# Kernel tuning notes

Hardware: AMD Instinct MI355X
Metric: run time of the kernel (lower is better)

The kernel has to match this reference:

```python
import math
import jax, jax.numpy as jnp
import numpy as np

BATCH, DEPTH = 16, 12
N_NODES = 2 ** DEPTH - 1  # 4095, heap layout: children of i are 2i+1, 2i+2
IN_F, OUT_F, STATE_F = 512, 512, 256


def setup_inputs() -> dict:
    key = jax.random.key(0)
    ks = jax.random.split(key, 10)
    x_batch = jax.random.normal(ks[0], (BATCH, N_NODES, IN_F), dtype=jnp.float32)
    idx_batch = jnp.arange(BATCH, dtype=jnp.int32)
    W_in = jax.random.normal(ks[1], (IN_F, IN_F), dtype=jnp.float32) / math.sqrt(IN_F)
    b_in = jnp.zeros((IN_F,), dtype=jnp.float32)
    u1 = jax.random.uniform(ks[2], (STATE_F,), dtype=jnp.float32)
    u2 = jax.random.uniform(ks[3], (STATE_F,), dtype=jnp.float32)
    nu_log = jnp.log(-0.5 * jnp.log(u1 + 1e-6))
    theta_log = jnp.log(2.0 * math.pi * u2)
    lam_mod = jnp.exp(-jnp.exp(nu_log))
    gamma_log = jnp.log(jnp.sqrt(1.0 - jnp.square(lam_mod)))
    B_re = jax.random.normal(ks[4], (STATE_F, IN_F), dtype=jnp.float32) / math.sqrt(2 * IN_F)
    B_im = jax.random.normal(ks[5], (STATE_F, IN_F), dtype=jnp.float32) / math.sqrt(2 * IN_F)
    C_re = jax.random.normal(ks[6], (OUT_F, STATE_F), dtype=jnp.float32) / math.sqrt(STATE_F)
    C_im = jax.random.normal(ks[7], (OUT_F, STATE_F), dtype=jnp.float32) / math.sqrt(STATE_F)
    return dict(x_batch=x_batch, idx_batch=idx_batch, W_in=W_in, b_in=b_in,
                nu_log=nu_log, theta_log=theta_log, gamma_log=gamma_log,
                B_re=B_re, B_im=B_im, C_re=C_re, C_im=C_im)


def reference(x_batch, idx_batch, W_in, b_in, nu_log, theta_log, gamma_log,
              B_re, B_im, C_re, C_im):
    bsz, n_nodes, _ = x_batch.shape
    depth = int(round(math.log2(n_nodes + 1)))
    S = B_re.shape[0]

    # LRU constants (complex lambda kept as (re, im) pair)
    lam_mod = jnp.exp(-jnp.exp(nu_log))           # [S]
    th = jnp.exp(theta_log)
    lr, li = lam_mod * jnp.cos(th), lam_mod * jnp.sin(th)
    gamma = jnp.exp(gamma_log)                    # [S]

    proj = x_batch @ W_in.T + b_in                # [B, N, IN]
    # complex input term (proj is real): proj @ B^T
    in_re = jnp.einsum('bni,si->bns', proj, B_re) # [B, N, S]
    in_im = jnp.einsum('bni,si->bns', proj, B_im)

    h_re = jnp.zeros((bsz, n_nodes, S), dtype=proj.dtype)
    h_im = jnp.zeros((bsz, n_nodes, S), dtype=proj.dtype)

    # process levels bottom-up; level d nodes occupy [2^d-1, 2^{d+1}-1)
    for d in range(depth - 1, -1, -1):
        a, b = 2 ** d - 1, 2 ** (d + 1) - 1
        n = b - a
        if d == depth - 1:  # leaves: left/right = -1 -> zero child state
            cr = jnp.zeros((bsz, n, S), dtype=proj.dtype)
            ci = jnp.zeros((bsz, n, S), dtype=proj.dtype)
        else:
            # children of nodes [a, b) are the contiguous block [2a+1, 2b+1)
            cr = h_re[:, 2 * a + 1:2 * b + 1].reshape(bsz, n, 2, S).sum(axis=2)
            ci = h_im[:, 2 * a + 1:2 * b + 1].reshape(bsz, n, 2, S).sum(axis=2)
        hr = lr * cr - li * ci + gamma * in_re[:, a:b]
        hi = lr * ci + li * cr + gamma * in_im[:, a:b]
        h_re = h_re.at[:, a:b].set(hr)
        h_im = h_im.at[:, a:b].set(hi)

    # y = Re(h @ C^T), computed once on final states (same math as per-level scatter)
    outputs = jnp.einsum('bns,os->bno', h_re, C_re) - jnp.einsum('bns,os->bno', h_im, C_im)
    return outputs
```

## Files before the change

kernel.cpp:

```cpp
#include <hip/hip_runtime.h>


#define ROWS 65520
#define KDIM 512

typedef __attribute__((ext_vector_type(8))) short bf16x8;
typedef __attribute__((ext_vector_type(4))) float f32x4;

__device__ __forceinline__ unsigned short f2bf(float f) {
    unsigned int u = __float_as_uint(f);
    unsigned int r = (u + 0x7FFFu + ((u >> 16) & 1u)) >> 16;
    return (unsigned short)r;
}
__device__ __forceinline__ float b2f(unsigned short h) {
    return __uint_as_float(((unsigned int)h) << 16);
}

#define CVT_BLKS  32760
#define PM_BASE   32760
#define PC_BASE   33784
#define PB_BASE   34808
#define PREP_GRID 34936

__global__ __launch_bounds__(256) void prep_all(const float* __restrict__ x,
                                                unsigned short* __restrict__ x16,
                                                const float* __restrict__ W,
                                                const float* __restrict__ Bre,
                                                const float* __restrict__ Bim,
                                                const float* __restrict__ gamma_log,
                                                unsigned short* __restrict__ M16,
                                                const float* __restrict__ bin,
                                                float* __restrict__ biasc,
                                                const float* __restrict__ Cre,
                                                const float* __restrict__ Cim,
                                                unsigned short* __restrict__ C16) {
    __shared__ float Bs[16][17];
    __shared__ float Ws[16][17];
    const int blk = blockIdx.x;
    const int t = threadIdx.x;

    if (blk < CVT_BLKS) {
        int i = blk * 256 + t;
        float4 v = ((const float4*)x)[i];
        ushort4 o;
        o.x = f2bf(v.x); o.y = f2bf(v.y); o.z = f2bf(v.z); o.w = f2bf(v.w);
        ((ushort4*)x16)[i] = o;
    } else if (blk < PC_BASE) {
        const int pm = blk - PM_BASE;
        const int bx = pm & 31;
        const int by = pm >> 5;
        const int tx = t & 15;
        const int ty = t >> 4;
        const int j  = bx * 16 + tx;
        const int cc = by * 16 + ty;
        const float* Bsel = (cc < 256) ? (Bre + (size_t)cc * 512)
                                       : (Bim + (size_t)(cc - 256) * 512);
        float acc = 0.f;
        for (int kt = 0; kt < 512; kt += 16) {
            Bs[ty][tx] = Bsel[kt + tx];
            Ws[ty][tx] = W[(size_t)(kt + ty) * 512 + j];
            __syncthreads();
#pragma unroll
            for (int k = 0; k < 16; ++k) acc += Bs[ty][k] * Ws[k][tx];
            __syncthreads();
        }
        float g = expf(gamma_log[cc & 255]);
        M16[(size_t)cc * 512 + j] = f2bf(acc * g);
    } else if (blk < PB_BASE) {
        int idx = (blk - PC_BASE) * 256 + t;
        int o = idx >> 9;
        int s = idx & 511;
        float v = (s < 256) ? Cre[(size_t)o * 256 + s] : -Cim[(size_t)o * 256 + (s - 256)];
        C16[idx] = f2bf(v);
    } else {
        const int c = (blk - PB_BASE) * 4 + (t >> 6);
        const int lane = t & 63;
        const float* Bsel = (c < 256) ? (Bre + (size_t)c * 512)
                                      : (Bim + (size_t)(c - 256) * 512);
        float acc = 0.f;
#pragma unroll
        for (int i = lane; i < 512; i += 64) acc += bin[i] * Bsel[i];
#pragma unroll
        for (int off = 32; off > 0; off >>= 1) acc += __shfl_down(acc, off, 64);
        if (lane == 0) biasc[c] = acc * expf(gamma_log[c & 255]);
    }
}

template <bool OUT_BF16>
__global__ __launch_bounds__(256) void gemm_mfma(const unsigned short* __restrict__ A,
                                                 const unsigned short* __restrict__ Bm,
                                                 const float* __restrict__ bias,
                                                 void* __restrict__ Cout,
                                                 int Mrows) {
    __shared__ __align__(16) unsigned short As[2][128 * 64];
    __shared__ __align__(16) unsigned short Bs[2][128 * 64];
    const int t = threadIdx.x;
    const int lane = t & 63;
    const int w = t >> 6;
    const int wr = (w >> 1) * 64;
    const int wc = (w & 1) * 64;
    const int bid = blockIdx.x;
    const int xcd = bid & 7;
    const int lid = bid >> 3;
    const int rowblk = xcd * 64 + (lid >> 2);
    const int colblk = lid & 3;
    const int row0 = rowblk * 128;
    const int col0 = colblk * 128;
    const int kt0  = (rowblk & 7) * 64;

    f32x4 acc[4][4] = {};

#define STAGE(pb, itv)                                                         \
    do {                                                                       \
        const int kt_ = (kt0 + (itv) * 64) & 511;                              \
        _Pragma("unroll")                                                      \
        for (int q = 0; q < 4; ++q) {                                          \
            int c_   = q * 256 + t;                                            \
            int row_ = c_ >> 3;                                                \
            int kc_  = c_ & 7;                                                 \
            int kg_  = kc_ ^ (row_ & 7);                                       \
            int ar_  = row0 + row_; if (ar_ >= Mrows) ar_ = Mrows - 1;         \
            const unsigned short* ga_ = A + (size_t)ar_ * KDIM + kt_ + kg_ * 8;\
            __builtin_amdgcn_global_load_lds(                                  \
                (const __attribute__((address_space(1))) unsigned int*)ga_,    \
                (__attribute__((address_space(3))) unsigned int*)(&As[pb][c_ * 8]),\
                16, 0, 0);                                                     \
            const unsigned short* gb_ = Bm + (size_t)(col0 + row_) * KDIM + kt_ + kg_ * 8;\
            __builtin_amdgcn_global_load_lds(                                  \
                (const __attribute__((address_space(1))) unsigned int*)gb_,    \
                (__attribute__((address_space(3))) unsigned int*)(&Bs[pb][c_ * 8]),\
                16, 0, 0);                                                     \
        }                                                                      \
    } while (0)

    STAGE(0, 0);
    __syncthreads();

    int cur = 0;
    for (int it = 0; it < 8; ++it) {
        if (it < 7) STAGE(cur ^ 1, it + 1);
#pragma unroll
        for (int kk = 0; kk < 64; kk += 32) {
            const int kgc = kk >> 3;
            bf16x8 af[4], bfr[4];
#pragma unroll
            for (int i = 0; i < 4; ++i) {
                int row = wr + i * 16 + (lane & 15);
                int kca = (kgc + (lane >> 4)) ^ (row & 7);
                af[i] = *(const bf16x8*)(&As[cur][row * 64 + kca * 8]);
                int colr = wc + i * 16 + (lane & 15);
                int kcb = (kgc + (lane >> 4)) ^ (colr & 7);
                bfr[i] = *(const bf16x8*)(&Bs[cur][colr * 64 + kcb * 8]);
            }
#pragma unroll
            for (int i = 0; i < 4; ++i)
#pragma unroll
                for (int j = 0; j < 4; ++j)
                    acc[i][j] = __builtin_amdgcn_mfma_f32_16x16x32_bf16(
                        af[i], bfr[j], acc[i][j], 0, 0, 0);
        }
        __syncthreads();
        cur ^= 1;
    }
#undef STAGE

    const int cq = lane >> 4;
    const int cl = lane & 15;
#pragma unroll
    for (int i = 0; i < 4; ++i) {
#pragma unroll
        for (int j = 0; j < 4; ++j) {
#pragma unroll
            for (int r = 0; r < 4; ++r) {
                int grow = row0 + wr + i * 16 + cq * 4 + r;
                int gcol = col0 + wc + j * 16 + cl;
                if (grow < Mrows) {
                    float v = acc[i][j][r];
                    if (bias) v += bias[gcol];
                    if (OUT_BF16)
                        ((unsigned short*)Cout)[(size_t)grow * 512 + gcol] = f2bf(v);
                    else
                        ((float*)Cout)[(size_t)grow * 512 + gcol] = v;
                }
            }
        }
    }
}

template <int E>
__global__ __launch_bounds__(256) void tree_up(unsigned short* __restrict__ buf,
                                               const float* __restrict__ nu_log,
                                               const float* __restrict__ theta_log,
                                               int root_base) {
    const int b = blockIdx.x;
    const int rs = root_base + blockIdx.y;
    const int c = threadIdx.x;
    constexpr int LEAVES = 1 << E;
    const float lam = expf(-expf(nu_log[c]));
    const float th  = expf(theta_log[c]);
    const float lr  = lam * cosf(th);
    const float li  = lam * sinf(th);
    const size_t base = (size_t)b * 4095;

    float vr[LEAVES], vi[LEAVES];
    {
        const int nbL = ((rs + 1) << E) - 1;
#pragma unroll
        for (int i = 0; i < LEAVES; ++i) {
            const size_t r = (base + nbL + i) * 512;
            vr[i] = b2f(buf[r + c]);
            vi[i] = b2f(buf[r + 256 + c]);
        }
    }
    float gr[LEAVES - 1], gi[LEAVES - 1];
    {
        int idx = 0;
#pragma unroll
        for (int e = E - 1; e >= 0; --e) {
            const int n  = 1 << e;
            const int nb = ((rs + 1) << e) - 1;
#pragma unroll
            for (int i = 0; i < n; ++i) {
                const size_t r = (base + nb + i) * 512;
                gr[idx] = b2f(buf[r + c]);
                gi[idx] = b2f(buf[r + 256 + c]);
                ++idx;
            }
        }
    }
    {
        int idx = 0;
#pragma unroll
        for (int e = E - 1; e >= 0; --e) {
            const int n  = 1 << e;
            const int nb = ((rs + 1) << e) - 1;
#pragma unroll
            for (int i = 0; i < n; ++i) {
                const float cr = vr[2 * i] + vr[2 * i + 1];
                const float ci = vi[2 * i] + vi[2 * i + 1];
                const float hr = lr * cr - li * ci + gr[idx];
                const float hi = lr * ci + li * cr + gi[idx];
                ++idx;
                const size_t r = (base + nb + i) * 512;
                buf[r + c]       = f2bf(hr);
                buf[r + 256 + c] = f2bf(hi);
                vr[i] = hr;
                vi[i] = hi;
            }
        }
    }
}

extern "C" void kernel_launch(void* const* d_in, const int* in_sizes, int n_in,
                              void* d_out, int out_size, void* d_ws, size_t ws_size,
                              hipStream_t stream) {
    const float* x         = (const float*)d_in[0];
    const float* W_in      = (const float*)d_in[2];
    const float* b_in      = (const float*)d_in[3];
    const float* nu_log    = (const float*)d_in[4];
    const float* theta_log = (const float*)d_in[5];
    const float* gamma_log = (const float*)d_in[6];
    const float* B_re      = (const float*)d_in[7];
    const float* B_im      = (const float*)d_in[8];
    const float* C_re      = (const float*)d_in[9];
    const float* C_im      = (const float*)d_in[10];
    float* out = (float*)d_out;

    char* ws = (char*)d_ws;
    const size_t HB = (size_t)ROWS * 512 * 2;
    unsigned short* x16   = (unsigned short*)ws;
    unsigned short* hb16  = (unsigned short*)(ws + HB);
    unsigned short* M16   = (unsigned short*)(ws + 2 * HB);
    unsigned short* C16   = (unsigned short*)(ws + 2 * HB + 512 * 512 * 2);
    float*          biasc = (float*)(ws + 2 * HB + 2 * 512 * 512 * 2);

    prep_all<<<PREP_GRID, 256, 0, stream>>>(x, x16, W_in, B_re, B_im, gamma_log,
                                            M16, b_in, biasc, C_re, C_im, C16);

    gemm_mfma<true><<<2048, 256, 0, stream>>>(x16, M16, biasc, hb16, ROWS);

    tree_up<4><<<dim3(16, 128), 256, 0, stream>>>(hb16, nu_log, theta_log, 127);
    tree_up<4><<<dim3(16, 8),   256, 0, stream>>>(hb16, nu_log, theta_log, 7);
    tree_up<3><<<dim3(16, 1),   256, 0, stream>>>(hb16, nu_log, theta_log, 0);

    gemm_mfma<false><<<2048, 256, 0, stream>>>(hb16, C16, nullptr, out, ROWS);
}
```

Measured before the change: 413.5 us.

## Vectorize tree scan loads, grid-stride x conversion, hoist GEMM addresses, setprio

```diff
diff --git a/kernel.cpp b/kernel.cpp
--- a/kernel.cpp
+++ b/kernel.cpp
@@ -15,12 +15,19 @@
 __device__ __forceinline__ float b2f(unsigned short h) {
     return __uint_as_float(((unsigned int)h) << 16);
 }
-
-#define CVT_BLKS  32760
-#define PM_BASE   32760
-#define PC_BASE   33784
-#define PB_BASE   34808
-#define PREP_GRID 34936
+__device__ __forceinline__ float b2f_lo(unsigned int p) {
+    return __uint_as_float(p << 16);
+}
+__device__ __forceinline__ float b2f_hi(unsigned int p) {
+    return __uint_as_float(p & 0xFFFF0000u);
+}
+
+#define PC_BASE   1024
+#define PB_BASE   2048
+#define CVT_BASE  2176
+#define CVT_BLKS  2048
+#define PREP_GRID 4224
+#define CVT_N4    8386560
 
 __global__ __launch_bounds__(256) void prep_all(const float* __restrict__ x,
                                                 unsigned short* __restrict__ x16,
@@ -39,16 +46,9 @@
     const int blk = blockIdx.x;
     const int t = threadIdx.x;
 
-    if (blk < CVT_BLKS) {
-        int i = blk * 256 + t;
-        float4 v = ((const float4*)x)[i];
-        ushort4 o;
-        o.x = f2bf(v.x); o.y = f2bf(v.y); o.z = f2bf(v.z); o.w = f2bf(v.w);
-        ((ushort4*)x16)[i] = o;
-    } else if (blk < PC_BASE) {
-        const int pm = blk - PM_BASE;
-        const int bx = pm & 31;
-        const int by = pm >> 5;
+    if (blk < PC_BASE) {
+        const int bx = blk & 31;
+        const int by = blk >> 5;
         const int tx = t & 15;
         const int ty = t >> 4;
         const int j  = bx * 16 + tx;
@@ -72,7 +72,7 @@
         int s = idx & 511;
         float v = (s < 256) ? Cre[(size_t)o * 256 + s] : -Cim[(size_t)o * 256 + (s - 256)];
         C16[idx] = f2bf(v);
-    } else {
+    } else if (blk < CVT_BASE) {
         const int c = (blk - PB_BASE) * 4 + (t >> 6);
         const int lane = t & 63;
         const float* Bsel = (c < 256) ? (Bre + (size_t)c * 512)
@@ -83,6 +83,15 @@
 #pragma unroll
         for (int off = 32; off > 0; off >>= 1) acc += __shfl_down(acc, off, 64);
         if (lane == 0) biasc[c] = acc * expf(gamma_log[c & 255]);
+    } else {
+        int i = (blk - CVT_BASE) * 256 + t;
+#pragma unroll 4
+        for (; i < CVT_N4; i += CVT_BLKS * 256) {
+            float4 v = ((const float4*)x)[i];
+            ushort4 o;
+            o.x = f2bf(v.x); o.y = f2bf(v.y); o.z = f2bf(v.z); o.w = f2bf(v.w);
+            ((ushort4*)x16)[i] = o;
+        }
     }
 }
 
@@ -110,25 +119,33 @@
 
     f32x4 acc[4][4] = {};
 
+    const unsigned short* gaB[4];
+    const unsigned short* gbB[4];
+    int ldsoff[4];
+#pragma unroll
+    for (int q = 0; q < 4; ++q) {
+        int c_   = q * 256 + t;
+        int row_ = c_ >> 3;
+        int kc_  = c_ & 7;
+        int kg_  = kc_ ^ (row_ & 7);
+        int ar_  = row0 + row_; if (ar_ >= Mrows) ar_ = Mrows - 1;
+        gaB[q] = A + (size_t)ar_ * KDIM + kg_ * 8;
+        gbB[q] = Bm + (size_t)(col0 + row_) * KDIM + kg_ * 8;
+        ldsoff[q] = c_ * 8;
+    }
+
 #define STAGE(pb, itv)                                                         \
     do {                                                                       \
         const int kt_ = (kt0 + (itv) * 64) & 511;                              \
         _Pragma("unroll")                                                      \
         for (int q = 0; q < 4; ++q) {                                          \
-            int c_   = q * 256 + t;                                            \
-            int row_ = c_ >> 3;                                                \
-            int kc_  = c_ & 7;                                                 \
-            int kg_  = kc_ ^ (row_ & 7);                                       \
-            int ar_  = row0 + row_; if (ar_ >= Mrows) ar_ = Mrows - 1;         \
-            const unsigned short* ga_ = A + (size_t)ar_ * KDIM + kt_ + kg_ * 8;\
             __builtin_amdgcn_global_load_lds(                                  \
-                (const __attribute__((address_space(1))) unsigned int*)ga_,    \
-                (__attribute__((address_space(3))) unsigned int*)(&As[pb][c_ * 8]),\
+                (const __attribute__((address_space(1))) unsigned int*)(gaB[q] + kt_),\
+                (__attribute__((address_space(3))) unsigned int*)(&As[pb][ldsoff[q]]),\
                 16, 0, 0);                                                     \
-            const unsigned short* gb_ = Bm + (size_t)(col0 + row_) * KDIM + kt_ + kg_ * 8;\
             __builtin_amdgcn_global_load_lds(                                  \
-                (const __attribute__((address_space(1))) unsigned int*)gb_,    \
-                (__attribute__((address_space(3))) unsigned int*)(&Bs[pb][c_ * 8]),\
+                (const __attribute__((address_space(1))) unsigned int*)(gbB[q] + kt_),\
+                (__attribute__((address_space(3))) unsigned int*)(&Bs[pb][ldsoff[q]]),\
                 16, 0, 0);                                                     \
         }                                                                      \
     } while (0)
@@ -139,6 +156,7 @@
     int cur = 0;
     for (int it = 0; it < 8; ++it) {
         if (it < 7) STAGE(cur ^ 1, it + 1);
+        __builtin_amdgcn_s_setprio(1);
 #pragma unroll
         for (int kk = 0; kk < 64; kk += 32) {
             const int kgc = kk >> 3;
@@ -159,6 +177,7 @@
                     acc[i][j] = __builtin_amdgcn_mfma_f32_16x16x32_bf16(
                         af[i], bfr[j], acc[i][j], 0, 0, 0);
         }
+        __builtin_amdgcn_s_setprio(0);
         __syncthreads();
         cur ^= 1;
     }
@@ -188,65 +207,72 @@
 }
 
 template <int E>
-__global__ __launch_bounds__(256) void tree_up(unsigned short* __restrict__ buf,
-                                               const float* __restrict__ nu_log,
-                                               const float* __restrict__ theta_log,
-                                               int root_base) {
+__global__ __launch_bounds__(256) void tree_up2(unsigned short* __restrict__ buf,
+                                                const float* __restrict__ nu_log,
+                                                const float* __restrict__ theta_log,
+                                                int root_base, int nroots) {
     const int b = blockIdx.x;
-    const int rs = root_base + blockIdx.y;
-    const int c = threadIdx.x;
+    const int h = threadIdx.x >> 7;
+    const int j2 = (threadIdx.x & 127) * 2;
+    const int rr = blockIdx.y * 2 + h;
+    if (rr >= nroots) return;
+    const int rs = root_base + rr;
     constexpr int LEAVES = 1 << E;
-    const float lam = expf(-expf(nu_log[c]));
-    const float th  = expf(theta_log[c]);
-    const float lr  = lam * cosf(th);
-    const float li  = lam * sinf(th);
+    constexpr int NODES = LEAVES - 1;
+
+    float lr0, li0, lr1, li1;
+    { const float lam = expf(-expf(nu_log[j2]));     const float th = expf(theta_log[j2]);
+      lr0 = lam * cosf(th); li0 = lam * sinf(th); }
+    { const float lam = expf(-expf(nu_log[j2 + 1])); const float th = expf(theta_log[j2 + 1]);
+      lr1 = lam * cosf(th); li1 = lam * sinf(th); }
     const size_t base = (size_t)b * 4095;
 
-    float vr[LEAVES], vi[LEAVES];
-    {
-        const int nbL = ((rs + 1) << E) - 1;
-#pragma unroll
-        for (int i = 0; i < LEAVES; ++i) {
-            const size_t r = (base + nbL + i) * 512;
-            vr[i] = b2f(buf[r + c]);
-            vi[i] = b2f(buf[r + 256 + c]);
-        }
-    }
-    float gr[LEAVES - 1], gi[LEAVES - 1];
-    {
-        int idx = 0;
-#pragma unroll
-        for (int e = E - 1; e >= 0; --e) {
-            const int n  = 1 << e;
-            const int nb = ((rs + 1) << e) - 1;
-#pragma unroll
-            for (int i = 0; i < n; ++i) {
-                const size_t r = (base + nb + i) * 512;
-                gr[idx] = b2f(buf[r + c]);
-                gi[idx] = b2f(buf[r + 256 + c]);
-                ++idx;
-            }
-        }
-    }
-    {
-        int idx = 0;
-#pragma unroll
-        for (int e = E - 1; e >= 0; --e) {
-            const int n  = 1 << e;
-            const int nb = ((rs + 1) << e) - 1;
-#pragma unroll
-            for (int i = 0; i < n; ++i) {
-                const float cr = vr[2 * i] + vr[2 * i + 1];
-                const float ci = vi[2 * i] + vi[2 * i + 1];
-                const float hr = lr * cr - li * ci + gr[idx];
-                const float hi = lr * ci + li * cr + gi[idx];
-                ++idx;
-                const size_t r = (base + nb + i) * 512;
-                buf[r + c]       = f2bf(hr);
-                buf[r + 256 + c] = f2bf(hi);
-                vr[i] = hr;
-                vi[i] = hi;
-            }
+    unsigned int pr[LEAVES], pi[LEAVES];
+    const int nbL = ((rs + 1) << E) - 1;
+#pragma unroll
+    for (int i = 0; i < LEAVES; ++i) {
+        const size_t r = (base + nbL + i) * 512;
+        pr[i] = *(const unsigned int*)(buf + r + j2);
+        pi[i] = *(const unsigned int*)(buf + r + 256 + j2);
+    }
+    unsigned int qr[NODES], qi[NODES];
+#pragma unroll
+    for (int e = E - 1; e >= 0; --e) {
+#pragma unroll
+        for (int i = 0; i < (1 << e); ++i) {
+            const int idx = LEAVES - (2 << e) + i;
+            const size_t r = (base + (((rs + 1) << e) - 1) + i) * 512;
+            qr[idx] = *(const unsigned int*)(buf + r + j2);
+            qi[idx] = *(const unsigned int*)(buf + r + 256 + j2);
+        }
+    }
+    __builtin_amdgcn_sched_barrier(0);
+
+    float vr0[LEAVES], vi0[LEAVES], vr1[LEAVES], vi1[LEAVES];
+#pragma unroll
+    for (int i = 0; i < LEAVES; ++i) {
+        vr0[i] = b2f_lo(pr[i]); vr1[i] = b2f_hi(pr[i]);
+        vi0[i] = b2f_lo(pi[i]); vi1[i] = b2f_hi(pi[i]);
+    }
+#pragma unroll
+    for (int e = E - 1; e >= 0; --e) {
+#pragma unroll
+        for (int i = 0; i < (1 << e); ++i) {
+            const int idx = LEAVES - (2 << e) + i;
+            const float cr0 = vr0[2 * i] + vr0[2 * i + 1];
+            const float ci0 = vi0[2 * i] + vi0[2 * i + 1];
+            const float cr1 = vr1[2 * i] + vr1[2 * i + 1];
+            const float ci1 = vi1[2 * i] + vi1[2 * i + 1];
+            const float hr0 = lr0 * cr0 - li0 * ci0 + b2f_lo(qr[idx]);
+            const float hi0 = lr0 * ci0 + li0 * cr0 + b2f_lo(qi[idx]);
+            const float hr1 = lr1 * cr1 - li1 * ci1 + b2f_hi(qr[idx]);
+            const float hi1 = lr1 * ci1 + li1 * cr1 + b2f_hi(qi[idx]);
+            const size_t r = (base + (((rs + 1) << e) - 1) + i) * 512;
+            *(unsigned int*)(buf + r + j2) =
+                (unsigned int)f2bf(hr0) | ((unsigned int)f2bf(hr1) << 16);
+            *(unsigned int*)(buf + r + 256 + j2) =
+                (unsigned int)f2bf(hi0) | ((unsigned int)f2bf(hi1) << 16);
+            vr0[i] = hr0; vi0[i] = hi0; vr1[i] = hr1; vi1[i] = hi1;
         }
     }
 }
@@ -279,9 +305,9 @@
 
     gemm_mfma<true><<<2048, 256, 0, stream>>>(x16, M16, biasc, hb16, ROWS);
 
-    tree_up<4><<<dim3(16, 128), 256, 0, stream>>>(hb16, nu_log, theta_log, 127);
-    tree_up<4><<<dim3(16, 8),   256, 0, stream>>>(hb16, nu_log, theta_log, 7);
-    tree_up<3><<<dim3(16, 1),   256, 0, stream>>>(hb16, nu_log, theta_log, 0);
+    tree_up2<4><<<dim3(16, 64), 256, 0, stream>>>(hb16, nu_log, theta_log, 127, 128);
+    tree_up2<4><<<dim3(16, 4),  256, 0, stream>>>(hb16, nu_log, theta_log, 7, 8);
+    tree_up2<3><<<dim3(16, 1),  256, 0, stream>>>(hb16, nu_log, theta_log, 0, 1);
 
     gemm_mfma<false><<<2048, 256, 0, stream>>>(hb16, C16, nullptr, out, ROWS);
 }
```

Result: faster. 399.9 us (-3.3%).
